# Performance work log

Measured on AMD Instinct MI355X. Metric: run time of the kernel, lower is better.

The kernel has to match this reference:

```python
import math
import jax, jax.numpy as jnp
import numpy as np

N, L, D = 64, 128, 768          # batch, n_in capsules, feature dim
IN_DIM, OUT_DIM, N_OUT = 64, 64, 32
EPS = 1e-8

def _xavier(k, shape):
    # torch xavier_uniform: fan_in = shape[1]*prod(shape[2:]), fan_out = shape[0]*prod(shape[2:])
    rec = int(np.prod(shape[2:])) if len(shape) > 2 else 1
    fan_in, fan_out = shape[-2] * rec, shape[-1] * rec
    a = math.sqrt(6.0 / (fan_in + fan_out))
    return jax.random.uniform(k, shape, jnp.float32, -a, a)

def setup_inputs() -> dict:
    key = jax.random.key(0)
    ks = jax.random.split(key, 4)
    return {
        "x": jax.random.normal(ks[0], (N, L, D), jnp.float32),
        "Wscore": _xavier(ks[1], (L, D, 1)),
        "Bscore": jnp.zeros((L, 1, 1), jnp.float32),
        "Wcap": _xavier(ks[2], (L, D, IN_DIM)),
        "Bcap": jnp.zeros((L, 1, IN_DIM), jnp.float32),
        "Wvote": _xavier(ks[3], (L, N_OUT, IN_DIM, OUT_DIM)),
        "Bvote": jnp.zeros((L, N_OUT, 1, OUT_DIM), jnp.float32),
        "beta_use": jnp.zeros((L, 1, 1, 1), jnp.float32),
        "beta_ign": jnp.zeros((1, N_OUT, 1, 1), jnp.float32),
        "iters": 3,
    }

def reference(x, Wscore, Bscore, Wcap, Bcap, Wvote, Bvote, beta_use, beta_ign, iters):
    n_out = Wvote.shape[1]
    pi = jnp.asarray(math.pi, x.dtype)
    x_t = jnp.transpose(x, (1, 0, 2))                     # (L, N, D)
    a_in = jnp.matmul(x_t, Wscore) + Bscore               # (L, N, 1)
    mu_in = jax.nn.gelu(jnp.matmul(x_t, Wcap) + Bcap, approximate=False)  # (L, N, in_dim)
    f_a_in = jax.nn.sigmoid(a_in)[:, None, :, :]          # (L, 1, N, 1)
    # votes: (L, n_out, N, out_dim)
    V = jnp.einsum('lni,loij->lonj', mu_in, Wvote) + Bvote

    def em_step(R):
        D_use = f_a_in * R                                # (L, n_out, N, 1)
        D_ign = f_a_in - D_use
        a_out = jnp.sum(beta_use * D_use, axis=0) - jnp.sum(beta_ign * D_ign, axis=0)  # (n_out, N, 1)
        denom = jnp.sum(D_use, axis=0) + EPS              # (n_out, N, 1)
        mu_out = jnp.sum(D_use * V, axis=0) / denom       # (n_out, N, out_dim)
        var_out = jnp.sum(D_use * (V - mu_out[None]) ** 2, axis=0) / denom
        return a_out, mu_out, var_out

    R = jnp.full((1, n_out, 1, 1), 1.0 / n_out, dtype=x.dtype)
    a_out, mu_out, var_out = em_step(R)
    for _ in range(int(iters) - 1):
        # Gaussian log-likelihood of each vote under each output capsule
        log_p = (-jnp.sum((V - mu_out[None]) ** 2 / (2.0 * var_out[None] + EPS), axis=-1)
                 - 1.0 - 0.5 * pi
                 - 0.5 * jnp.sum(jnp.log(var_out[None] + EPS), axis=-1))   # (L, n_out, N)
        R = jax.nn.softmax(jax.nn.log_sigmoid(a_out)[None] + log_p[..., None], axis=1)
        a_out, mu_out, var_out = em_step(R)

    a_out = jnp.transpose(a_out[..., 0], (1, 0))          # (N, n_out)
    mu_out = jnp.transpose(mu_out, (1, 0, 2))             # (N, n_out, out_dim)
    return a_out, mu_out
```

## Files before the change

kernel.cpp:

```cpp
#include <hip/hip_runtime.h>
#include <math.h>

#define NB 64
#define LL 128
#define DD 768
#define ID 64
#define OD 64
#define NO 32
#define EPSF 1e-8f

typedef unsigned short ushort_t;
typedef __attribute__((ext_vector_type(8))) short bf16x8;
typedef __attribute__((ext_vector_type(4))) float f32x4;


__device__ __forceinline__ float gelu_exact(float v) {
  return 0.5f * v * (1.0f + erff(v * 0.70710678118654752440f));
}
__device__ __forceinline__ float sigmoidf_(float z) {
  return 1.0f / (1.0f + __expf(-z));
}
__device__ __forceinline__ unsigned short f2bf(float f) {
  unsigned u = __float_as_uint(f);
  unsigned r = (u + 0x7FFFu + ((u >> 16) & 1u)) >> 16;
  return (unsigned short)r;
}
__device__ __forceinline__ float bf2f(unsigned short s) {
  return __uint_as_float(((unsigned)s) << 16);
}

__global__ __launch_bounds__(256) void k0a_proj(
    const float* __restrict__ x, const float* __restrict__ Wscore,
    const float* __restrict__ Wcap,
    float* __restrict__ Cpart, float* __restrict__ apart)
{
  const int l  = blockIdx.x & 127;
  const int kc = blockIdx.x >> 7;
  const int t = threadIdx.x;
  const int tn = t >> 4;
  const int ti = t & 15;
  __shared__ float Xs[64][68];
  __shared__ float Ws[64][68];
  __shared__ float Ss[64];
  float C[4][4] = {{0.f}};
  float asum[4] = {0.f, 0.f, 0.f, 0.f};

  for (int kt = 0; kt < 2; ++kt) {
    const int kbase = kc * 128 + kt * 64;
#pragma unroll
    for (int r = 0; r < 4; ++r) {
      const int flat = r * 1024 + t * 4;
      const int p = flat >> 6, qq = flat & 63;
      *(float4*)&Xs[p][qq] = *(const float4*)&x[(p * LL + l) * DD + kbase + qq];
      *(float4*)&Ws[p][qq] = *(const float4*)&Wcap[(l * DD + kbase + p) * ID + qq];
    }
    if (t < 16)
      *(float4*)&Ss[4 * t] = *(const float4*)&Wscore[l * DD + kbase + 4 * t];
    __syncthreads();
#pragma unroll 8
    for (int k = 0; k < 64; ++k) {
      float av[4];
      av[0] = Xs[4 * tn + 0][k];
      av[1] = Xs[4 * tn + 1][k];
      av[2] = Xs[4 * tn + 2][k];
      av[3] = Xs[4 * tn + 3][k];
      const float4 b = *(const float4*)&Ws[k][4 * ti];
      const float sk = Ss[k];
#pragma unroll
      for (int a = 0; a < 4; ++a) {
        C[a][0] = fmaf(av[a], b.x, C[a][0]);
        C[a][1] = fmaf(av[a], b.y, C[a][1]);
        C[a][2] = fmaf(av[a], b.z, C[a][2]);
        C[a][3] = fmaf(av[a], b.w, C[a][3]);
        asum[a] = fmaf(av[a], sk, asum[a]);
      }
    }
    __syncthreads();
  }
#pragma unroll
  for (int a = 0; a < 4; ++a)
    *(float4*)&Cpart[kc * 524288 + (l * 64 + 4 * tn + a) * 64 + 4 * ti] =
        make_float4(C[a][0], C[a][1], C[a][2], C[a][3]);
  if (ti == 0) {
#pragma unroll
    for (int a = 0; a < 4; ++a)
      apart[kc * 8192 + l * 64 + 4 * tn + a] = asum[a];
  }
}

__global__ __launch_bounds__(256) void k0b_reduce(
    const float* __restrict__ Cpart, const float* __restrict__ Bcap,
    ushort_t* __restrict__ Ah, ushort_t* __restrict__ Al)
{
  const int e = (blockIdx.x * 256 + threadIdx.x) * 4;
  float4 s = *(const float4*)&Cpart[e];
#pragma unroll
  for (int kc = 1; kc < 6; ++kc) {
    const float4 p = *(const float4*)&Cpart[kc * 524288 + e];
    s.x += p.x; s.y += p.y; s.z += p.z; s.w += p.w;
  }
  const int l = e >> 12;
  const int n = (e >> 6) & 63;
  const int i0 = e & 63;
  const float4 bc = *(const float4*)&Bcap[l * 64 + i0];
  float m[4] = {gelu_exact(s.x + bc.x), gelu_exact(s.y + bc.y),
                gelu_exact(s.z + bc.z), gelu_exact(s.w + bc.w)};
  ushort4 h, lo;
  h.x = f2bf(m[0]); lo.x = f2bf(m[0] - bf2f(h.x));
  h.y = f2bf(m[1]); lo.y = f2bf(m[1] - bf2f(h.y));
  h.z = f2bf(m[2]); lo.z = f2bf(m[2] - bf2f(h.z));
  h.w = f2bf(m[3]); lo.w = f2bf(m[3] - bf2f(h.w));
  const int off = l * 4096 + (i0 >> 5) * 2048 + (n >> 4) * 512 + (n & 15) * 32 +
                  ((i0 >> 3) & 3) * 8 + (i0 & 7);
  *(ushort4*)&Ah[off] = h;
  *(ushort4*)&Al[off] = lo;
}

__global__ __launch_bounds__(256) void k0c_fa(
    const float* __restrict__ apart, const float* __restrict__ Bscore,
    float* __restrict__ f_a)
{
  const int e = blockIdx.x * 256 + threadIdx.x;
  float s = 0.f;
#pragma unroll
  for (int kc = 0; kc < 6; ++kc) s += apart[kc * 8192 + e];
  const int l = e >> 6;
  f_a[e] = sigmoidf_(s + Bscore[l]);
}

__global__ __launch_bounds__(256) void k1_votes(
    const ushort_t* __restrict__ Ah, const ushort_t* __restrict__ Al,
    const float* __restrict__ Wvote, const float* __restrict__ Bvote,
    float* __restrict__ V)
{
  const int t = threadIdx.x;
  const int w = t >> 6;
  const int lane = t & 63;
  const int g = blockIdx.x * 4 + w;
  const int pair = g >> 1;
  const int jh = g & 1;
  const int l = pair >> 5;
  const int mr = lane & 15, q = lane >> 4;

  __shared__ unsigned HL_all[4][1024];
  unsigned* HL = HL_all[w];

  const float* Wt = Wvote + (size_t)pair * 4096 + jh * 32;
  const int afoff = mr * 32 + q * 8;

  float bv[2];
#pragma unroll
  for (int nt = 0; nt < 2; ++nt)
    bv[nt] = Bvote[pair * 64 + jh * 32 + 16 * nt + mr];

  f32x4 acc[4][2];
#pragma unroll
  for (int mt = 0; mt < 4; ++mt)
#pragma unroll
    for (int nt = 0; nt < 2; ++nt) {
      f32x4 z = {0.f, 0.f, 0.f, 0.f};
      acc[mt][nt] = z;
    }

#pragma unroll 1
  for (int ks = 0; ks < 2; ++ks) {
#pragma unroll
    for (int f = 0; f < 4; ++f) {
      const int idx = f * 64 + lane;
      const int r = idx >> 3;
      const int c4 = (idx & 7) * 4;
      const float4 v4 = *(const float4*)&Wt[ks * 2048 + r * 64 + c4];
      const int jc = c4 ^ ((r & 8) << 1);
      const float e4[4] = {v4.x, v4.y, v4.z, v4.w};
      unsigned pk[4];
#pragma unroll
      for (int d = 0; d < 4; ++d) {
        const unsigned short hi = f2bf(e4[d]);
        const unsigned short lo = f2bf(e4[d] - bf2f(hi));
        pk[d] = (unsigned)hi | ((unsigned)lo << 16);
      }
      *(uint4*)&HL[r * 32 + jc] = make_uint4(pk[0], pk[1], pk[2], pk[3]);
    }

    bf16x8 afh[4], afl[4];
#pragma unroll
    for (int mt = 0; mt < 4; ++mt) {
      const int off = l * 4096 + ks * 2048 + mt * 512 + afoff;
      afh[mt] = *(const bf16x8*)&Ah[off];
      afl[mt] = *(const bf16x8*)&Al[off];
    }

#pragma unroll
    for (int nt = 0; nt < 2; ++nt) {
      const int j = 16 * nt + mr;
      unsigned wv[8];
#pragma unroll
      for (int d = 0; d < 8; ++d) {
        const int ii = q * 8 + d;
        wv[d] = HL[ii * 32 + (j ^ ((ii & 8) << 1))];
      }
      union { ushort_t u[8]; bf16x8 v; } bh, bl;
#pragma unroll
      for (int d = 0; d < 8; ++d) {
        bh.u[d] = (ushort_t)(wv[d] & 0xffffu);
        bl.u[d] = (ushort_t)(wv[d] >> 16);
      }
#pragma unroll
      for (int mt = 0; mt < 4; ++mt) {
        acc[mt][nt] = __builtin_amdgcn_mfma_f32_16x16x32_bf16(
            afh[mt], bh.v, acc[mt][nt], 0, 0, 0);
        acc[mt][nt] = __builtin_amdgcn_mfma_f32_16x16x32_bf16(
            afh[mt], bl.v, acc[mt][nt], 0, 0, 0);
        acc[mt][nt] = __builtin_amdgcn_mfma_f32_16x16x32_bf16(
            afl[mt], bh.v, acc[mt][nt], 0, 0, 0);
      }
    }
  }

  float* T = (float*)HL;
#pragma unroll
  for (int mt = 0; mt < 4; ++mt) {
#pragma unroll
    for (int nt = 0; nt < 2; ++nt)
#pragma unroll
      for (int r = 0; r < 4; ++r)
        T[(4 * q + r) * 36 + 16 * nt + mr] = acc[mt][nt][r] + bv[nt];
#pragma unroll
    for (int rr = 0; rr < 2; ++rr) {
      const int row = rr * 8 + (lane >> 3);
      const int c4e = (lane & 7) * 4;
      const float4 vv = *(const float4*)&T[row * 36 + c4e];
      const size_t base = (size_t)(16 * mt + row) * (LL * NO * OD) +
                          (size_t)pair * 64 + jh * 32 + c4e;
      *(float4*)&V[base] = vv;
    }
  }
}

__global__ __launch_bounds__(256) void k3_em(
    const float* __restrict__ V, const float* __restrict__ f_a,
    const float* __restrict__ beta_use, const float* __restrict__ mu_s,
    const float* __restrict__ i2v_s, const float* __restrict__ cterm,
    float* __restrict__ S1p, float* __restrict__ S2p,
    float* __restrict__ dnp, float* __restrict__ aUp, const int mode)
{
  const int n = blockIdx.x >> 3;
  const int c = blockIdx.x & 7;
  const int t = threadIdx.x;
  const int o = t >> 3, q = t & 7;
  __shared__ float ttl[8][32];

  float mu8[8], iv8[8];
  float ct = 0.f;
  if (mode) {
    const float4 a0 = *(const float4*)&mu_s[n * 2048 + t * 8];
    const float4 a1 = *(const float4*)&mu_s[n * 2048 + t * 8 + 4];
    mu8[0] = a0.x; mu8[1] = a0.y; mu8[2] = a0.z; mu8[3] = a0.w;
    mu8[4] = a1.x; mu8[5] = a1.y; mu8[6] = a1.z; mu8[7] = a1.w;
    const float4 b0 = *(const float4*)&i2v_s[n * 2048 + t * 8];
    const float4 b1 = *(const float4*)&i2v_s[n * 2048 + t * 8 + 4];
    iv8[0] = b0.x; iv8[1] = b0.y; iv8[2] = b0.z; iv8[3] = b0.w;
    iv8[4] = b1.x; iv8[5] = b1.y; iv8[6] = b1.z; iv8[7] = b1.w;
    ct = cterm[n * NO + o];
  }
  float aS1[8] = {0.f, 0.f, 0.f, 0.f, 0.f, 0.f, 0.f, 0.f};
  float aS2[8] = {0.f, 0.f, 0.f, 0.f, 0.f, 0.f, 0.f, 0.f};
  float dn = 0.f, aU = 0.f;

  const float* Vb = V + (size_t)n * LL * 2048 + t * 8;

  float VA[4][8], VB[4][8], faA[4], faB[4], buA[4], buB[4];

  auto LOAD = [&](float (&Vv)[4][8], float (&fa4)[4], float (&bu4)[4],
                  const int g) {
    const int lb = c * 16 + g * 4;
#pragma unroll
    for (int u = 0; u < 4; ++u) {
      const int l = lb + u;
      const float4 v0 = *(const float4*)&Vb[(size_t)l * 2048];
      const float4 v1 = *(const float4*)&Vb[(size_t)l * 2048 + 4];
      Vv[u][0] = v0.x; Vv[u][1] = v0.y; Vv[u][2] = v0.z; Vv[u][3] = v0.w;
      Vv[u][4] = v1.x; Vv[u][5] = v1.y; Vv[u][6] = v1.z; Vv[u][7] = v1.w;
      fa4[u] = f_a[l * NB + n];
      bu4[u] = beta_use[l];
    }
  };

  auto COMP = [&](float (&Vv)[4][8], float (&fa4)[4], float (&bu4)[4],
                  const int g) {
    if (mode) {
      float tt4[4];
#pragma unroll
      for (int u = 0; u < 4; ++u) {
        float s2 = 0.f;
#pragma unroll
        for (int k = 0; k < 8; ++k) {
          const float d = Vv[u][k] - mu8[k];
          s2 = fmaf(d * d, iv8[k], s2);
        }
        s2 += __shfl_xor(s2, 1);
        s2 += __shfl_xor(s2, 2);
        s2 += __shfl_xor(s2, 4);
        tt4[u] = ct - s2;
      }
      const int sb = (g & 1) * 4;
      if (q == 0) {
#pragma unroll
        for (int u = 0; u < 4; ++u) ttl[sb + u][o] = tt4[u];
      }
      __syncthreads();
#pragma unroll
      for (int u = 0; u < 4; ++u) {
        const float vv = ttl[sb + u][t & 31];
        float m = vv;
#pragma unroll
        for (int msk = 1; msk <= 16; msk <<= 1) m = fmaxf(m, __shfl_xor(m, msk));
        float z = __expf(vv - m);
#pragma unroll
        for (int msk = 1; msk <= 16; msk <<= 1) z += __shfl_xor(z, msk);
        const float wgt = fa4[u] * __expf(tt4[u] - m) / z;
        dn += wgt;
        aU = fmaf(bu4[u], wgt, aU);
#pragma unroll
        for (int k = 0; k < 8; ++k) {
          const float d = Vv[u][k] - mu8[k];
          aS1[k] = fmaf(wgt, Vv[u][k], aS1[k]);
          aS2[k] = fmaf(wgt, d * d, aS2[k]);
        }
      }
    } else {
#pragma unroll
      for (int u = 0; u < 4; ++u) {
        const float wgt = fa4[u] * (1.0f / NO);
        dn += wgt;
        aU = fmaf(bu4[u], wgt, aU);
#pragma unroll
        for (int k = 0; k < 8; ++k) {
          aS1[k] = fmaf(wgt, Vv[u][k], aS1[k]);
          aS2[k] = fmaf(wgt * Vv[u][k], Vv[u][k], aS2[k]);
        }
      }
    }
  };

  LOAD(VA, faA, buA, 0);
  LOAD(VB, faB, buB, 1);
  COMP(VA, faA, buA, 0);
  LOAD(VA, faA, buA, 2);
  COMP(VB, faB, buB, 1);
  LOAD(VB, faB, buB, 3);
  COMP(VA, faA, buA, 2);
  COMP(VB, faB, buB, 3);

  const int base = ((c * NB + n) * NO + o) * OD + q * 8;
  *(float4*)&S1p[base]     = make_float4(aS1[0], aS1[1], aS1[2], aS1[3]);
  *(float4*)&S1p[base + 4] = make_float4(aS1[4], aS1[5], aS1[6], aS1[7]);
  *(float4*)&S2p[base]     = make_float4(aS2[0], aS2[1], aS2[2], aS2[3]);
  *(float4*)&S2p[base + 4] = make_float4(aS2[4], aS2[5], aS2[6], aS2[7]);
  if (q == 0) {
    dnp[(c * NB + n) * NO + o] = dn;
    aUp[(c * NB + n) * NO + o] = aU;
  }
}

__global__ __launch_bounds__(64) void k4_fin23(
    const float* __restrict__ S1p, const float* __restrict__ S2p,
    const float* __restrict__ dnp, const float* __restrict__ aUp,
    const float* __restrict__ f_a, const float* __restrict__ beta_ign,
    float* __restrict__ mu_s, float* __restrict__ i2v_s, float* __restrict__ cterm,
    float* __restrict__ out, const int final_iter, const int first)
{
  const int n = blockIdx.x >> 5;
  const int o = blockIdx.x & 31;
  const int j = threadIdx.x;

  float fs = f_a[j * NB + n] + f_a[(j + 64) * NB + n];
#pragma unroll
  for (int msk = 32; msk >= 1; msk >>= 1) fs += __shfl_xor(fs, msk);
  const float Fsum = fs;

  float dn = 0.f, aU = 0.f;
#pragma unroll
  for (int cc = 0; cc < 8; ++cc) {
    dn += dnp[(cc * NB + n) * NO + o];
    aU += aUp[(cc * NB + n) * NO + o];
  }
  const float S0 = dn;
  const float denom = dn + EPSF;
  const float inv_den = 1.0f / denom;

  float S1 = 0.f, S2 = 0.f;
#pragma unroll
  for (int cc = 0; cc < 8; ++cc) {
    const int base = ((cc * NB + n) * NO + o) * OD + j;
    S1 += S1p[base];
    S2 += S2p[base];
  }
  const float mup = first ? 0.f : mu_s[n * 2048 + o * 64 + j];
  const float aout = aU - beta_ign[o] * (Fsum - dn);

  const float mu = S1 * inv_den;
  const float dd = mu - mup;
  const float varn = S2 - 2.0f * dd * (S1 - mup * S0) + dd * dd * S0;
  const float var = fmaxf(varn * inv_den, 0.0f);
  const float i2v = 1.0f / (2.0f * var + EPSF);

  if (final_iter) {
    if (j == 0) out[n * NO + o] = aout;
    out[2048 + n * 2048 + o * 64 + j] = mu;
  } else {
    mu_s[n * 2048 + o * 64 + j] = mu;
    i2v_s[n * 2048 + o * 64 + j] = i2v;
    float lacc = logf(var + EPSF);
#pragma unroll
    for (int msk = 32; msk >= 1; msk >>= 1) lacc += __shfl_xor(lacc, msk);
    if (j == 0) {
      const float lsg = fminf(aout, 0.0f) - log1pf(__expf(-fabsf(aout)));
      cterm[n * NO + o] = lsg - 0.5f * lacc;
    }
  }
}

extern "C" void kernel_launch(void* const* d_in, const int* in_sizes, int n_in,
                              void* d_out, int out_size, void* d_ws, size_t ws_size,
                              hipStream_t stream) {
  const float* x        = (const float*)d_in[0];
  const float* Wscore   = (const float*)d_in[1];
  const float* Bscore   = (const float*)d_in[2];
  const float* Wcap     = (const float*)d_in[3];
  const float* Bcap     = (const float*)d_in[4];
  const float* Wvote    = (const float*)d_in[5];
  const float* Bvote    = (const float*)d_in[6];
  const float* beta_use = (const float*)d_in[7];
  const float* beta_ign = (const float*)d_in[8];
  float* out = (float*)d_out;

  float* ws     = (float*)d_ws;
  float* V      = ws;
  float* Cpart  = ws;
  float* apart  = ws + 3145728;
  ushort_t* Ah  = (ushort_t*)(ws + 16777216);
  ushort_t* Al  = Ah + 524288;
  float* f_a    = ws + 16777216 + 524288;
  float* S1p    = f_a + 8192;
  float* S2p    = S1p + 1048576;
  float* dnp    = S2p + 1048576;
  float* aUp    = dnp + 16384;
  float* mu_s   = aUp + 16384;
  float* i2v_s  = mu_s + 131072;
  float* ct     = i2v_s + 131072;
  const size_t need = (size_t)(16777216 + 524288 + 8192 + 2 * 1048576 +
                               2 * 16384 + 2 * 131072 + 2048) * sizeof(float);
  if (ws_size < need) return;

  k0a_proj<<<768, 256, 0, stream>>>(x, Wscore, Wcap, Cpart, apart);
  k0b_reduce<<<512, 256, 0, stream>>>(Cpart, Bcap, Ah, Al);
  k0c_fa<<<32, 256, 0, stream>>>(apart, Bscore, f_a);
  k1_votes<<<2048, 256, 0, stream>>>(Ah, Al, Wvote, Bvote, V);
  k3_em<<<512, 256, 0, stream>>>(V, f_a, beta_use, mu_s, i2v_s, ct, S1p, S2p, dnp, aUp, 0);
  k4_fin23<<<2048, 64, 0, stream>>>(S1p, S2p, dnp, aUp, f_a, beta_ign, mu_s, i2v_s, ct, out, 0, 1);
  k3_em<<<512, 256, 0, stream>>>(V, f_a, beta_use, mu_s, i2v_s, ct, S1p, S2p, dnp, aUp, 1);
  k4_fin23<<<2048, 64, 0, stream>>>(S1p, S2p, dnp, aUp, f_a, beta_ign, mu_s, i2v_s, ct, out, 0, 0);
  k3_em<<<512, 256, 0, stream>>>(V, f_a, beta_use, mu_s, i2v_s, ct, S1p, S2p, dnp, aUp, 1);
  k4_fin23<<<2048, 64, 0, stream>>>(S1p, S2p, dnp, aUp, f_a, beta_ign, mu_s, i2v_s, ct, out, 1, 0);
}
```

Baseline: 242.2 us.

## Fuse EM finalize into EM kernels via last-block atomic counter; merge reduce kernels

Merges the f_a sigmoid kernel into the Cpart reduction kernel and removes the separate finalize kernels. Each EM pass now has the last of the 8 chunk blocks per batch item, detected with an atomic counter and threadfence, compute mu, var, i2v and cterm. The final pass also skips computing and storing the unused second-moment partials. This cuts launch count and kernel-boundary gaps, in exchange for a serialized tail on the last block and reliance on correct fence and counter semantics.

New measurement: 329.7 us. 36.1% more time.

```diff
diff --git a/kernel.cpp b/kernel.cpp
--- a/kernel.cpp
+++ b/kernel.cpp
@@ -88,11 +88,15 @@
   }
 }
 
-__global__ __launch_bounds__(256) void k0b_reduce(
+__global__ __launch_bounds__(256) void k0bc(
     const float* __restrict__ Cpart, const float* __restrict__ Bcap,
-    ushort_t* __restrict__ Ah, ushort_t* __restrict__ Al)
+    const float* __restrict__ apart, const float* __restrict__ Bscore,
+    ushort_t* __restrict__ Ah, ushort_t* __restrict__ Al,
+    float* __restrict__ f_a, int* __restrict__ cnt)
 {
-  const int e = (blockIdx.x * 256 + threadIdx.x) * 4;
+  const int bid = blockIdx.x;
+  const int t = threadIdx.x;
+  const int e = (bid * 256 + t) * 4;
   float4 s = *(const float4*)&Cpart[e];
 #pragma unroll
   for (int kc = 1; kc < 6; ++kc) {
@@ -114,18 +118,15 @@
                   ((i0 >> 3) & 3) * 8 + (i0 & 7);
   *(ushort4*)&Ah[off] = h;
   *(ushort4*)&Al[off] = lo;
-}
-
-__global__ __launch_bounds__(256) void k0c_fa(
-    const float* __restrict__ apart, const float* __restrict__ Bscore,
-    float* __restrict__ f_a)
-{
-  const int e = blockIdx.x * 256 + threadIdx.x;
-  float s = 0.f;
-#pragma unroll
-  for (int kc = 0; kc < 6; ++kc) s += apart[kc * 8192 + e];
-  const int l = e >> 6;
-  f_a[e] = sigmoidf_(s + Bscore[l]);
+
+  if (bid < 32) {
+    const int e2 = bid * 256 + t;
+    float ss = 0.f;
+#pragma unroll
+    for (int kc = 0; kc < 6; ++kc) ss += apart[kc * 8192 + e2];
+    f_a[e2] = sigmoidf_(ss + Bscore[e2 >> 6]);
+  }
+  if (bid == 32 && t < 64) cnt[t] = 0;
 }
 
 __global__ __launch_bounds__(256) void k1_votes(
@@ -237,22 +238,27 @@
   }
 }
 
-__global__ __launch_bounds__(256) void k3_em(
+template <int MODE>
+__global__ __launch_bounds__(256) void k3f_em(
     const float* __restrict__ V, const float* __restrict__ f_a,
-    const float* __restrict__ beta_use, const float* __restrict__ mu_s,
-    const float* __restrict__ i2v_s, const float* __restrict__ cterm,
+    const float* __restrict__ beta_use, const float* __restrict__ beta_ign,
+    float* __restrict__ mu_s, float* __restrict__ i2v_s,
+    float* __restrict__ cterm,
     float* __restrict__ S1p, float* __restrict__ S2p,
-    float* __restrict__ dnp, float* __restrict__ aUp, const int mode)
+    float* __restrict__ dnp, float* __restrict__ aUp,
+    float* __restrict__ out, int* __restrict__ cnt)
 {
   const int n = blockIdx.x >> 3;
   const int c = blockIdx.x & 7;
   const int t = threadIdx.x;
   const int o = t >> 3, q = t & 7;
   __shared__ float ttl[8][32];
+  __shared__ float rA[128];
+  __shared__ int lastFlag;
 
   float mu8[8], iv8[8];
   float ct = 0.f;
-  if (mode) {
+  if (MODE != 0) {
     const float4 a0 = *(const float4*)&mu_s[n * 2048 + t * 8];
     const float4 a1 = *(const float4*)&mu_s[n * 2048 + t * 8 + 4];
     mu8[0] = a0.x; mu8[1] = a0.y; mu8[2] = a0.z; mu8[3] = a0.w;
@@ -288,7 +294,7 @@
 
   auto COMP = [&](float (&Vv)[4][8], float (&fa4)[4], float (&bu4)[4],
                   const int g) {
-    if (mode) {
+    if (MODE != 0) {
       float tt4[4];
 #pragma unroll
       for (int u = 0; u < 4; ++u) {
@@ -323,9 +329,11 @@
         aU = fmaf(bu4[u], wgt, aU);
 #pragma unroll
         for (int k = 0; k < 8; ++k) {
-          const float d = Vv[u][k] - mu8[k];
           aS1[k] = fmaf(wgt, Vv[u][k], aS1[k]);
-          aS2[k] = fmaf(wgt, d * d, aS2[k]);
+          if (MODE != 2) {
+            const float d = Vv[u][k] - mu8[k];
+            aS2[k] = fmaf(wgt, d * d, aS2[k]);
+          }
         }
       }
     } else {
@@ -355,68 +363,91 @@
   const int base = ((c * NB + n) * NO + o) * OD + q * 8;
   *(float4*)&S1p[base]     = make_float4(aS1[0], aS1[1], aS1[2], aS1[3]);
   *(float4*)&S1p[base + 4] = make_float4(aS1[4], aS1[5], aS1[6], aS1[7]);
-  *(float4*)&S2p[base]     = make_float4(aS2[0], aS2[1], aS2[2], aS2[3]);
-  *(float4*)&S2p[base + 4] = make_float4(aS2[4], aS2[5], aS2[6], aS2[7]);
+  if (MODE != 2) {
+    *(float4*)&S2p[base]     = make_float4(aS2[0], aS2[1], aS2[2], aS2[3]);
+    *(float4*)&S2p[base + 4] = make_float4(aS2[4], aS2[5], aS2[6], aS2[7]);
+  }
   if (q == 0) {
     dnp[(c * NB + n) * NO + o] = dn;
     aUp[(c * NB + n) * NO + o] = aU;
   }
-}
-
-__global__ __launch_bounds__(64) void k4_fin23(
-    const float* __restrict__ S1p, const float* __restrict__ S2p,
-    const float* __restrict__ dnp, const float* __restrict__ aUp,
-    const float* __restrict__ f_a, const float* __restrict__ beta_ign,
-    float* __restrict__ mu_s, float* __restrict__ i2v_s, float* __restrict__ cterm,
-    float* __restrict__ out, const int final_iter, const int first)
-{
-  const int n = blockIdx.x >> 5;
-  const int o = blockIdx.x & 31;
-  const int j = threadIdx.x;
-
-  float fs = f_a[j * NB + n] + f_a[(j + 64) * NB + n];
-#pragma unroll
-  for (int msk = 32; msk >= 1; msk >>= 1) fs += __shfl_xor(fs, msk);
-  const float Fsum = fs;
-
-  float dn = 0.f, aU = 0.f;
-#pragma unroll
-  for (int cc = 0; cc < 8; ++cc) {
-    dn += dnp[(cc * NB + n) * NO + o];
-    aU += aUp[(cc * NB + n) * NO + o];
-  }
-  const float S0 = dn;
-  const float denom = dn + EPSF;
-  const float inv_den = 1.0f / denom;
-
-  float S1 = 0.f, S2 = 0.f;
-#pragma unroll
-  for (int cc = 0; cc < 8; ++cc) {
-    const int base = ((cc * NB + n) * NO + o) * OD + j;
-    S1 += S1p[base];
-    S2 += S2p[base];
-  }
-  const float mup = first ? 0.f : mu_s[n * 2048 + o * 64 + j];
-  const float aout = aU - beta_ign[o] * (Fsum - dn);
-
-  const float mu = S1 * inv_den;
-  const float dd = mu - mup;
-  const float varn = S2 - 2.0f * dd * (S1 - mup * S0) + dd * dd * S0;
-  const float var = fmaxf(varn * inv_den, 0.0f);
-  const float i2v = 1.0f / (2.0f * var + EPSF);
-
-  if (final_iter) {
-    if (j == 0) out[n * NO + o] = aout;
-    out[2048 + n * 2048 + o * 64 + j] = mu;
-  } else {
-    mu_s[n * 2048 + o * 64 + j] = mu;
-    i2v_s[n * 2048 + o * 64 + j] = i2v;
-    float lacc = logf(var + EPSF);
-#pragma unroll
-    for (int msk = 32; msk >= 1; msk >>= 1) lacc += __shfl_xor(lacc, msk);
-    if (j == 0) {
-      const float lsg = fminf(aout, 0.0f) - log1pf(__expf(-fabsf(aout)));
-      cterm[n * NO + o] = lsg - 0.5f * lacc;
+
+  __syncthreads();
+  if (t == 0) {
+    __threadfence();
+    const int old = atomicAdd(&cnt[n], 1);
+    lastFlag = (old == MODE * 8 + 7) ? 1 : 0;
+  }
+  __syncthreads();
+  if (lastFlag) {
+    __threadfence();
+
+    if (t < 128) rA[t] = f_a[t * NB + n];
+    __syncthreads();
+    for (int s = 64; s >= 1; s >>= 1) {
+      if (t < s) rA[t] += rA[t + s];
+      __syncthreads();
+    }
+    const float Fsum = rA[0];
+
+    float dnF = 0.f, aUF = 0.f;
+#pragma unroll
+    for (int cc = 0; cc < 8; ++cc) {
+      dnF += dnp[(cc * NB + n) * NO + o];
+      aUF += aUp[(cc * NB + n) * NO + o];
+    }
+    const float S0 = dnF;
+    const float inv_den = 1.0f / (dnF + EPSF);
+
+    float S1v[8], S2v[8];
+#pragma unroll
+    for (int k = 0; k < 8; ++k) { S1v[k] = 0.f; S2v[k] = 0.f; }
+    for (int cc = 0; cc < 8; ++cc) {
+      const int b2 = ((cc * NB + n) * NO + o) * OD + q * 8;
+      const float4 u0 = *(const float4*)&S1p[b2];
+      const float4 u1 = *(const float4*)&S1p[b2 + 4];
+      S1v[0] += u0.x; S1v[1] += u0.y; S1v[2] += u0.z; S1v[3] += u0.w;
+      S1v[4] += u1.x; S1v[5] += u1.y; S1v[6] += u1.z; S1v[7] += u1.w;
+      if (MODE != 2) {
+        const float4 w0 = *(const float4*)&S2p[b2];
+        const float4 w1 = *(const float4*)&S2p[b2 + 4];
+        S2v[0] += w0.x; S2v[1] += w0.y; S2v[2] += w0.z; S2v[3] += w0.w;
+        S2v[4] += w1.x; S2v[5] += w1.y; S2v[6] += w1.z; S2v[7] += w1.w;
+      }
+    }
+    const float aout = aUF - beta_ign[o] * (Fsum - dnF);
+
+    if (MODE == 2) {
+      if (q == 0) out[n * NO + o] = aout;
+      float muv[8];
+#pragma unroll
+      for (int k = 0; k < 8; ++k) muv[k] = S1v[k] * inv_den;
+      *(float4*)&out[2048 + n * 2048 + t * 8]     = make_float4(muv[0], muv[1], muv[2], muv[3]);
+      *(float4*)&out[2048 + n * 2048 + t * 8 + 4] = make_float4(muv[4], muv[5], muv[6], muv[7]);
+    } else {
+      float muv[8], i2vv[8];
+      float lacc = 0.f;
+#pragma unroll
+      for (int k = 0; k < 8; ++k) {
+        muv[k] = S1v[k] * inv_den;
+        const float mupk = (MODE == 0) ? 0.f : mu8[k];
+        const float dd = muv[k] - mupk;
+        const float varn = S2v[k] - 2.0f * dd * (S1v[k] - mupk * S0) + dd * dd * S0;
+        const float var = fmaxf(varn * inv_den, 0.0f);
+        i2vv[k] = 1.0f / (2.0f * var + EPSF);
+        lacc += logf(var + EPSF);
+      }
+      *(float4*)&mu_s[n * 2048 + t * 8]      = make_float4(muv[0], muv[1], muv[2], muv[3]);
+      *(float4*)&mu_s[n * 2048 + t * 8 + 4]  = make_float4(muv[4], muv[5], muv[6], muv[7]);
+      *(float4*)&i2v_s[n * 2048 + t * 8]     = make_float4(i2vv[0], i2vv[1], i2vv[2], i2vv[3]);
+      *(float4*)&i2v_s[n * 2048 + t * 8 + 4] = make_float4(i2vv[4], i2vv[5], i2vv[6], i2vv[7]);
+      lacc += __shfl_xor(lacc, 1);
+      lacc += __shfl_xor(lacc, 2);
+      lacc += __shfl_xor(lacc, 4);
+      if (q == 0) {
+        const float lsg = fminf(aout, 0.0f) - log1pf(__expf(-fabsf(aout)));
+        cterm[n * NO + o] = lsg - 0.5f * lacc;
+      }
     }
   }
 }
@@ -449,18 +480,18 @@
   float* mu_s   = aUp + 16384;
   float* i2v_s  = mu_s + 131072;
   float* ct     = i2v_s + 131072;
+  int*   cnt    = (int*)(ct + 2048);
   const size_t need = (size_t)(16777216 + 524288 + 8192 + 2 * 1048576 +
-                               2 * 16384 + 2 * 131072 + 2048) * sizeof(float);
+                               2 * 16384 + 2 * 131072 + 2048 + 64) * sizeof(float);
   if (ws_size < need) return;
 
   k0a_proj<<<768, 256, 0, stream>>>(x, Wscore, Wcap, Cpart, apart);
-  k0b_reduce<<<512, 256, 0, stream>>>(Cpart, Bcap, Ah, Al);
-  k0c_fa<<<32, 256, 0, stream>>>(apart, Bscore, f_a);
+  k0bc<<<512, 256, 0, stream>>>(Cpart, Bcap, apart, Bscore, Ah, Al, f_a, cnt);
   k1_votes<<<2048, 256, 0, stream>>>(Ah, Al, Wvote, Bvote, V);
-  k3_em<<<512, 256, 0, stream>>>(V, f_a, beta_use, mu_s, i2v_s, ct, S1p, S2p, dnp, aUp, 0);
-  k4_fin23<<<2048, 64, 0, stream>>>(S1p, S2p, dnp, aUp, f_a, beta_ign, mu_s, i2v_s, ct, out, 0, 1);
-  k3_em<<<512, 256, 0, stream>>>(V, f_a, beta_use, mu_s, i2v_s, ct, S1p, S2p, dnp, aUp, 1);
-  k4_fin23<<<2048, 64, 0, stream>>>(S1p, S2p, dnp, aUp, f_a, beta_ign, mu_s, i2v_s, ct, out, 0, 0);
-  k3_em<<<512, 256, 0, stream>>>(V, f_a, beta_use, mu_s, i2v_s, ct, S1p, S2p, dnp, aUp, 1);
-  k4_fin23<<<2048, 64, 0, stream>>>(S1p, S2p, dnp, aUp, f_a, beta_ign, mu_s, i2v_s, ct, out, 1, 0);
-}
+  k3f_em<0><<<512, 256, 0, stream>>>(V, f_a, beta_use, beta_ign, mu_s, i2v_s,
+                                     ct, S1p, S2p, dnp, aUp, out, cnt);
+  k3f_em<1><<<512, 256, 0, stream>>>(V, f_a, beta_use, beta_ign, mu_s, i2v_s,
+                                     ct, S1p, S2p, dnp, aUp, out, cnt);
+  k3f_em<2><<<512, 256, 0, stream>>>(V, f_a, beta_use, beta_ign, mu_s, i2v_s,
+                                     ct, S1p, S2p, dnp, aUp, out, cnt);
+}
```
